# Performance work log

Measured on AMD Instinct MI355X. Metric: run time of the kernel, lower is better.

The kernel has to match this reference:

```python
import math
import jax, jax.numpy as jnp
import numpy as np

H = 1024        # hidden_size
V = 32000       # target vocab
T = 64          # decoder steps
B = 32          # batch
NL = 2          # lstm layers
WSZ = 50        # window_size
WLEN = 2 * WSZ + 1
L = 128         # source length (all sequences full)
S = L + WLEN    # padded encoder length, guarantees windows in-bounds
HH = math.ceil(H / 2)
STD2 = (WSZ / 2.0) ** 2
EPS = 1e-14


def setup_inputs():
    key = jax.random.key(0)
    ks = jax.random.split(key, 16)
    sc = 0.02
    inp = {}
    inp["encoder_output"] = jax.random.normal(ks[0], (S, B, H), jnp.float32)
    inp["context"] = jax.random.normal(ks[1], (T, B, H), jnp.float32)
    inp["h0"] = jax.random.normal(ks[2], (NL, B, H), jnp.float32)
    inp["c0"] = jax.random.normal(ks[3], (NL, B, H), jnp.float32)
    inp["embedding"] = jax.random.normal(ks[4], (V, H), jnp.float32) * sc
    inp["attn_w1"] = jax.random.normal(ks[5], (HH, H), jnp.float32) * sc
    inp["attn_b1"] = jnp.zeros((HH,), jnp.float32)
    inp["attn_w2"] = jax.random.normal(ks[6], (1, HH), jnp.float32) * sc
    inp["attn_b2"] = jnp.zeros((1,), jnp.float32)
    inp["lstm_Wih0"] = jax.random.normal(ks[7], (4 * H, 2 * H), jnp.float32) * sc  # input feeding: 2H input
    inp["lstm_Whh0"] = jax.random.normal(ks[8], (4 * H, H), jnp.float32) * sc
    inp["lstm_bih0"] = jnp.zeros((4 * H,), jnp.float32)
    inp["lstm_bhh0"] = jnp.zeros((4 * H,), jnp.float32)
    inp["lstm_Wih1"] = jax.random.normal(ks[9], (4 * H, H), jnp.float32) * sc
    inp["lstm_Whh1"] = jax.random.normal(ks[10], (4 * H, H), jnp.float32) * sc
    inp["lstm_bih1"] = jnp.zeros((4 * H,), jnp.float32)
    inp["lstm_bhh1"] = jnp.zeros((4 * H,), jnp.float32)
    inp["fc1_w"] = jax.random.normal(ks[11], (H, 2 * H), jnp.float32) * sc
    inp["fc1_b"] = jnp.zeros((H,), jnp.float32)
    inp["fc2_w"] = jax.random.normal(ks[12], (V, H), jnp.float32) * sc
    inp["fc2_b"] = jnp.zeros((V,), jnp.float32)
    inp["target_words"] = jax.random.randint(ks[13], (T, B), 0, V)
    inp["lengths"] = jnp.full((B,), L, dtype=jnp.int32)
    return inp


def _lstm_layer(x, h0, c0, Wih, Whh, bih, bhh):
    bias = bih + bhh
    def step(carry, xt):
        h, c = carry
        gates = xt @ Wih.T + h @ Whh.T + bias   # [B, 4H], torch gate order i,f,g,o
        i, f, g, o = jnp.split(gates, 4, axis=-1)
        c = jax.nn.sigmoid(f) * c + jax.nn.sigmoid(i) * jnp.tanh(g)
        h = jax.nn.sigmoid(o) * jnp.tanh(c)
        return (h, c), h
    (hT, cT), ys = jax.lax.scan(step, (h0, c0), x)
    return ys, hT, cT


def _attention(encoder_output, dec_out, lengths, aw1, ab1, aw2, ab2):
    h_s = jnp.transpose(encoder_output, (1, 0, 2))   # [B, S, H]
    h_t = jnp.transpose(dec_out, (1, 0, 2))          # [B, T, H]
    p = jax.nn.sigmoid(jnp.tanh(h_t @ aw1.T + ab1) @ aw2.T + ab2)[..., 0]  # [B, T]
    p = WSZ + lengths[:, None].astype(jnp.float32) * p
    win_start = jnp.round(p - WSZ).astype(jnp.int32)                        # [B, T]
    k = jnp.arange(WLEN)
    positions = win_start[..., None].astype(jnp.float32) + k.astype(jnp.float32)  # [B, T, W]
    gaussian = jnp.exp(-((positions - p[..., None]) ** 2) / (2.0 * STD2))
    # faithful to original: the selection buffer is overwritten every j, so
    # every decoder step attends over the LAST step's window
    sel_idx = win_start[:, -1][:, None] + k                                 # [B, W]
    selection = jnp.take_along_axis(h_s, sel_idx[:, :, None], axis=1)       # [B, W, H]
    score = jnp.einsum('bth,bwh->btw', h_t, selection)
    li = lengths[:, None, None].astype(jnp.int32)
    lo = k[None, None, :] < (WSZ - win_start)[..., None]
    hi = k[None, None, :] >= (li + WSZ - win_start[..., None])
    score = jnp.where(lo | hi, EPS, score)   # original writes epsilon, NOT -inf
    a = jax.nn.softmax(score, axis=2) * gaussian
    c = jnp.einsum('btw,bwh->bth', a, selection)
    return jnp.transpose(c, (1, 0, 2))       # [T, B, H]


def reference(encoder_output, context, h0, c0, embedding,
              attn_w1, attn_b1, attn_w2, attn_b2,
              lstm_Wih0, lstm_Whh0, lstm_bih0, lstm_bhh0,
              lstm_Wih1, lstm_Whh1, lstm_bih1, lstm_bhh1,
              fc1_w, fc1_b, fc2_w, fc2_b,
              target_words, lengths):
    emb = embedding[target_words]                        # [T, B, H]
    x = jnp.concatenate([emb, context], axis=2)          # input feeding -> [T, B, 2H]
    y0, hT0, cT0 = _lstm_layer(x, h0[0], c0[0], lstm_Wih0, lstm_Whh0, lstm_bih0, lstm_bhh0)
    y1, hT1, cT1 = _lstm_layer(y0, h0[1], c0[1], lstm_Wih1, lstm_Whh1, lstm_bih1, lstm_bhh1)
    ctx = _attention(encoder_output, y1, lengths, attn_w1, attn_b1, attn_w2, attn_b2)
    out = jax.nn.relu(jnp.concatenate([ctx, y1], axis=2) @ fc1_w.T + fc1_b)
    y = out @ fc2_w.T + fc2_b                            # [T, B, V]
    h_n = jnp.stack([hT0, hT1])
    c_n = jnp.stack([cT0, cT1])
    return (y, h_n, c_n, ctx)
```

## Files before the change

kernel.cpp:

```cpp
#include <hip/hip_runtime.h>
#include <hip/hip_bf16.h>

#define T_STEPS 64
#define BATCH   32
#define HID     1024
#define VOCAB   32000
#define WLEN_   101
#define WSZ_    50
#define SENC    229
#define LBLK    64

static const size_t Y_SZ   = (size_t)T_STEPS * BATCH * VOCAB;
static const size_t HN_SZ  = (size_t)2 * BATCH * HID;
static const size_t CTX_OFF = Y_SZ + 2 * HN_SZ;

typedef __attribute__((ext_vector_type(8)))  unsigned short us8;
typedef __attribute__((ext_vector_type(8)))  __bf16 bf16x8;
typedef __attribute__((ext_vector_type(4)))  float f32x4;
typedef __attribute__((ext_vector_type(16))) float f32x16;

static __device__ inline unsigned short f2bf(float x) {
    __hip_bfloat16 b = __float2bfloat16(x);
    return __builtin_bit_cast(unsigned short, b);
}

#define GLD_US8_SC(dst, ptr) \
    asm volatile("global_load_dwordx4 %0, %1, off sc0 sc1" : "=v"(dst) : "v"(ptr) : "memory")
#define GLD_F32_SC(dst, ptr) \
    asm volatile("global_load_dword %0, %1, off sc0 sc1" : "=v"(dst) : "v"(ptr) : "memory")
#define GST_U16_SC(ptr, val) \
    asm volatile("global_store_short %0, %1, off sc0 sc1" :: "v"(ptr), "v"(val) : "memory")
#define GST_U32_SC(ptr, val) \
    asm volatile("global_store_dword %0, %1, off sc0 sc1" :: "v"(ptr), "v"(val) : "memory")
#define WAIT_VM0() asm volatile("s_waitcnt vmcnt(0)" ::: "memory")

__global__ __launch_bounds__(256) void gemm_bt(
    const float* __restrict__ A, const float* __restrict__ W,
    const float* __restrict__ b1, const float* __restrict__ b2,
    float* __restrict__ out, int M, int N, int K, int act)
{
    __shared__ __align__(16) float As[16 * 132];
    __shared__ __align__(16) float Ws[16 * 68];
    const int tid  = threadIdx.x;
    const int col0 = blockIdx.x * 64;
    const int row0 = blockIdx.y * 128;
    const int ty   = tid >> 4;
    const int tx   = tid & 15;

    float acc[8][4];
#pragma unroll
    for (int i = 0; i < 8; ++i)
#pragma unroll
        for (int j = 0; j < 4; ++j) acc[i][j] = 0.f;

    for (int k0 = 0; k0 < K; k0 += 16) {
#pragma unroll
        for (int li = 0; li < 2; ++li) {
            int f  = tid + li * 256;
            int r  = f >> 2;
            int kq = (f & 3) << 2;
            float4 v = *reinterpret_cast<const float4*>(A + (size_t)(row0 + r) * K + k0 + kq);
            As[(kq + 0) * 132 + r] = v.x;
            As[(kq + 1) * 132 + r] = v.y;
            As[(kq + 2) * 132 + r] = v.z;
            As[(kq + 3) * 132 + r] = v.w;
        }
        {
            int n  = tid >> 2;
            int kq = (tid & 3) << 2;
            float4 v = *reinterpret_cast<const float4*>(W + (size_t)(col0 + n) * K + k0 + kq);
            Ws[(kq + 0) * 68 + n] = v.x;
            Ws[(kq + 1) * 68 + n] = v.y;
            Ws[(kq + 2) * 68 + n] = v.z;
            Ws[(kq + 3) * 68 + n] = v.w;
        }
        __syncthreads();
#pragma unroll
        for (int k = 0; k < 16; ++k) {
            const float4 a0 = *reinterpret_cast<const float4*>(&As[k * 132 + ty * 8]);
            const float4 a1 = *reinterpret_cast<const float4*>(&As[k * 132 + ty * 8 + 4]);
            const float4 b0 = *reinterpret_cast<const float4*>(&Ws[k * 68 + tx * 4]);
            float av[8] = {a0.x, a0.y, a0.z, a0.w, a1.x, a1.y, a1.z, a1.w};
            float bv[4] = {b0.x, b0.y, b0.z, b0.w};
#pragma unroll
            for (int i = 0; i < 8; ++i)
#pragma unroll
                for (int j = 0; j < 4; ++j) acc[i][j] = fmaf(av[i], bv[j], acc[i][j]);
        }
        __syncthreads();
    }

#pragma unroll
    for (int j = 0; j < 4; ++j) {
        int n = col0 + tx * 4 + j;
        float bias = 0.f;
        if (b1) bias += b1[n];
        if (b2) bias += b2[n];
#pragma unroll
        for (int i = 0; i < 8; ++i) {
            float v = acc[i][j] + bias;
            if (act == 1) v = fmaxf(v, 0.f);
            else if (act == 2) v = tanhf(v);
            out[(size_t)(row0 + ty * 8 + i) * N + n] = v;
        }
    }
}

__global__ __launch_bounds__(256) void gemm_lds_bt(
    const unsigned short* __restrict__ A, const unsigned short* __restrict__ W,
    const float* __restrict__ b1, const float* __restrict__ b2,
    float* __restrict__ out, unsigned short* __restrict__ out_bf,
    int M, int N, int K, int relu)
{
    __shared__ __align__(16) unsigned short As[8192];
    __shared__ __align__(16) unsigned short Ws[8192];
    const int tid  = threadIdx.x;
    const int lane = tid & 63;
    const int wave = tid >> 6;

    const int nwg = gridDim.x;
    const int bid = blockIdx.x;
    const int q = nwg >> 3, r8 = nwg & 7;
    const int xcd = bid & 7, sidx = bid >> 3;
    const int wgid = (xcd < r8 ? xcd * (q + 1) : r8 * (q + 1) + (xcd - r8) * q) + sidx;
    const int mt = M >> 7;
    const int row0 = (wgid % mt) << 7;
    const int col0 = (wgid / mt) << 7;

    const int m0   = (wave >> 1) * 64;
    const int n0   = (wave & 1) * 64;
    const int lrow = lane & 15;
    const int kc   = lane >> 4;

    f32x4 acc[4][4];
#pragma unroll
    for (int i = 0; i < 4; ++i)
#pragma unroll
        for (int j = 0; j < 4; ++j) acc[i][j] = (f32x4){0.f, 0.f, 0.f, 0.f};

    const bool isA = (wave < 2);
    const int  lw  = wave & 1;
    const unsigned short* gbase = isA ? (A + (size_t)row0 * K) : (W + (size_t)col0 * K);
    unsigned short* lbase = isA ? As : Ws;

    for (int k0 = 0; k0 < K; k0 += 64) {
#pragma unroll
        for (int i = 0; i < 8; ++i) {
            const int c    = lw * 512 + i * 64 + lane;
            const int row  = c >> 3;
            const int slot = c & 7;
            const unsigned short* src =
                gbase + (size_t)row * K + k0 + ((slot ^ (row & 7)) << 3);
            __builtin_amdgcn_global_load_lds(
                (const __attribute__((address_space(1))) void*)src,
                (__attribute__((address_space(3))) void*)(lbase + (size_t)(lw * 512 + i * 64) * 8),
                16, 0, 0);
        }
        __syncthreads();
#pragma unroll
        for (int ss = 0; ss < 2; ++ss) {
            us8 a[4], b[4];
#pragma unroll
            for (int f = 0; f < 4; ++f) {
                const int ar = m0 + f * 16 + lrow;
                const int as = (ss * 4 + kc) ^ (ar & 7);
                a[f] = *reinterpret_cast<const us8*>(&As[(ar * 8 + as) * 8]);
                const int br = n0 + f * 16 + lrow;
                const int bs = (ss * 4 + kc) ^ (br & 7);
                b[f] = *reinterpret_cast<const us8*>(&Ws[(br * 8 + bs) * 8]);
            }
#pragma unroll
            for (int fi = 0; fi < 4; ++fi)
#pragma unroll
                for (int fj = 0; fj < 4; ++fj)
                    acc[fi][fj] = __builtin_amdgcn_mfma_f32_16x16x32_bf16(
                        __builtin_bit_cast(bf16x8, a[fi]),
                        __builtin_bit_cast(bf16x8, b[fj]),
                        acc[fi][fj], 0, 0, 0);
        }
        __syncthreads();
    }

#pragma unroll
    for (int fi = 0; fi < 4; ++fi)
#pragma unroll
        for (int fj = 0; fj < 4; ++fj) {
            const int cN = col0 + n0 + fj * 16 + lrow;
            float bv = 0.f;
            if (b1) bv += b1[cN];
            if (b2) bv += b2[cN];
#pragma unroll
            for (int j = 0; j < 4; ++j) {
                const int r = row0 + m0 + fi * 16 + (lane >> 4) * 4 + j;
                float v = acc[fi][fj][j] + bv;
                if (relu) v = fmaxf(v, 0.f);
                if (out)    out[(size_t)r * N + cN] = v;
                if (out_bf) out_bf[(size_t)r * N + cN] = f2bf(v);
            }
        }
}

__global__ void cvt_bf16_kernel(const float* __restrict__ src,
                                unsigned short* __restrict__ dst, int n8)
{
    for (int i = blockIdx.x * blockDim.x + threadIdx.x; i < n8;
         i += gridDim.x * blockDim.x) {
        float4 v0 = *reinterpret_cast<const float4*>(src + (size_t)i * 8);
        float4 v1 = *reinterpret_cast<const float4*>(src + (size_t)i * 8 + 4);
        us8 c = {f2bf(v0.x), f2bf(v0.y), f2bf(v0.z), f2bf(v0.w),
                 f2bf(v1.x), f2bf(v1.y), f2bf(v1.z), f2bf(v1.w)};
        *reinterpret_cast<us8*>(dst + (size_t)i * 8) = c;
    }
}

__global__ void embed_concat_bf_kernel(const float* __restrict__ emb,
                                       const float* __restrict__ ctxin,
                                       const int* __restrict__ tw,
                                       unsigned short* __restrict__ x_bf)
{
    const int total = 2048 * 256;
    for (int idx = blockIdx.x * blockDim.x + threadIdx.x; idx < total;
         idx += gridDim.x * blockDim.x) {
        int row = idx >> 8;
        int c8  = idx & 255;
        const float* src = (c8 < 128)
            ? emb + (size_t)tw[row] * HID + c8 * 8
            : ctxin + (size_t)row * HID + (c8 - 128) * 8;
        float4 v0 = *reinterpret_cast<const float4*>(src);
        float4 v1 = *reinterpret_cast<const float4*>(src + 4);
        us8 c = {f2bf(v0.x), f2bf(v0.y), f2bf(v0.z), f2bf(v0.w),
                 f2bf(v1.x), f2bf(v1.y), f2bf(v1.z), f2bf(v1.w)};
        *reinterpret_cast<us8*>(x_bf + (size_t)idx * 8) = c;
    }
}

__global__ void zero_flags_kernel(int* p, int n)
{
    int i = blockIdx.x * blockDim.x + threadIdx.x;
    if (i < n) p[i] = 0;
}

static __device__ inline void hier_arrive(int* __restrict__ flags, int phase, int tid)
{
    if (tid == 0)
        __hip_atomic_store(&flags[blockIdx.x * 32], phase,
                           __ATOMIC_RELAXED, __HIP_MEMORY_SCOPE_AGENT);
}

static __device__ inline void hier_wait(int* __restrict__ flags, int* __restrict__ epoch,
                                        int phase, int tid)
{
    if (blockIdx.x == 0) {
        if (tid < 3 * LBLK) {
            while (__hip_atomic_load(&flags[tid * 32], __ATOMIC_RELAXED,
                                     __HIP_MEMORY_SCOPE_AGENT) < phase)
                __builtin_amdgcn_s_sleep(1);
        }
        __syncthreads();
        if (tid < 8)
            __hip_atomic_store(&epoch[tid * 32], phase,
                               __ATOMIC_RELAXED, __HIP_MEMORY_SCOPE_AGENT);
    } else {
        if (tid == 0) {
            const int slot = (blockIdx.x & 7) * 32;
            while (__hip_atomic_load(&epoch[slot], __ATOMIC_RELAXED,
                                     __HIP_MEMORY_SCOPE_AGENT) < phase)
                __builtin_amdgcn_s_sleep(1);
        }
        __syncthreads();
    }
}

__global__ __launch_bounds__(256) void lstm_fused3(
    const float* __restrict__ gpre0,
    const float* __restrict__ Whh0, const float* __restrict__ Wih1,
    const float* __restrict__ Whh1,
    const float* __restrict__ bih1, const float* __restrict__ bhh1,
    const float* __restrict__ h0all, const float* __restrict__ c0all,
    float* __restrict__ y1o,
    unsigned short* __restrict__ fin_bf,
    float* __restrict__ hn, float* __restrict__ cn,
    unsigned short* __restrict__ hbf,
    float* __restrict__ part,
    int* __restrict__ flags, int* __restrict__ epoch,
    const float* __restrict__ fc2w, unsigned short* __restrict__ fc2w_bf,
    int foldcvt)
{
    __shared__ __align__(16) us8 WB[8192];
    __shared__ float red2[32 * 132];
    __shared__ float csh[512];

    const int tid  = threadIdx.x;
    const int lane = tid & 63;
    const int w    = tid >> 6;
    const int n    = lane & 31;
    const int kh   = lane >> 5;
    const int bid  = blockIdx.x;
    const int role = bid >> 6;
    const int lb   = bid & 63;
    const int j0   = lb * 16;
    const int b    = tid >> 3;
    const int jj   = tid & 7;

    unsigned short* hb0 = hbf;
    unsigned short* hb1 = hbf + 65536;

    {
        const float* Wsrc = (role == 0) ? Whh0 : (role == 1 ? Wih1 : Whh1);
        const int g = n >> 3, cj = n & 7;
#pragma unroll
        for (int T = 0; T < 2; ++T) {
            const float* wrow = Wsrc + (size_t)(g * HID + j0 + T * 8 + cj) * HID;
#pragma unroll
            for (int f = 0; f < 16; ++f) {
                int k = w * 256 + f * 16 + kh * 8;
                float4 v0 = *reinterpret_cast<const float4*>(wrow + k);
                float4 v1 = *reinterpret_cast<const float4*>(wrow + k + 4);
                WB[((T * 4 + w) * 16 + f) * 64 + lane] =
                    (us8){f2bf(v0.x), f2bf(v0.y), f2bf(v0.z), f2bf(v0.w),
                          f2bf(v1.x), f2bf(v1.y), f2bf(v1.z), f2bf(v1.w)};
            }
        }
    }

    float gp[2][4] = {};
    float bb[2][4] = {};
    if (role == 0) {
#pragma unroll
        for (int T = 0; T < 2; ++T) {
            csh[T * 256 + tid] = c0all[b * HID + j0 + T * 8 + jj];
#pragma unroll
            for (int g = 0; g < 4; ++g)
                gp[T][g] = gpre0[(size_t)b * 4096 + g * HID + j0 + T * 8 + jj];
        }
#pragma unroll
        for (int q = 0; q < 2; ++q) {
            int e = lb * 512 + q * 256 + tid;
            unsigned int hv = f2bf(h0all[((e >> 3) & 31) * HID + (e >> 8) * 8 + (e & 7)]);
            GST_U16_SC(hb0 + e, hv);
        }
    } else if (role == 2) {
#pragma unroll
        for (int T = 0; T < 2; ++T) {
            csh[T * 256 + tid] = c0all[32768 + b * HID + j0 + T * 8 + jj];
#pragma unroll
            for (int g = 0; g < 4; ++g)
                bb[T][g] = bih1[g * HID + j0 + T * 8 + jj] + bhh1[g * HID + j0 + T * 8 + jj];
        }
#pragma unroll
        for (int q = 0; q < 2; ++q) {
            int e = lb * 512 + q * 256 + tid;
            unsigned int hv = f2bf(h0all[32768 + ((e >> 3) & 31) * HID + (e >> 8) * 8 + (e & 7)]);
            GST_U16_SC(hb1 + 32768 + e, hv);
        }
    }

    WAIT_VM0();
    __syncthreads();
    hier_arrive(flags, 1, tid);
    hier_wait(flags, epoch, 1, tid);

    for (int p = 0; p <= 65; ++p) {
        const bool active = (role == 0) ? (p <= 63)
                          : (role == 1) ? (p >= 1 && p <= 64)
                                        : (p >= 2);
        if (active) {
            const int t = p - role;
            float pv[2][4];
            if (role == 2) {
                const float* pb = part + (size_t)(p & 1) * 131072 + lb * 2048 + tid;
#pragma unroll
                for (int T = 0; T < 2; ++T)
#pragma unroll
                    for (int g = 0; g < 4; ++g)
                        GLD_F32_SC(pv[T][g], pb + (T * 4 + g) * 256);
            }
            const unsigned short* hsrc = (role == 2)
                ? hb1 + ((p + 1) & 1) * 32768
                : hb0 + (p & 1) * 32768;
            const unsigned short* hr = hsrc + (size_t)w * 8192 + lane * 8;
            us8 aF[16];
#pragma unroll
            for (int f = 0; f < 16; ++f)
                GLD_US8_SC(aF[f], hr + f * 512);
            WAIT_VM0();
            __builtin_amdgcn_sched_barrier(0);

            f32x16 acc0 = {}, acc1 = {};
#pragma unroll
            for (int f = 0; f < 16; ++f)
                acc0 = __builtin_amdgcn_mfma_f32_32x32x16_bf16(
                    __builtin_bit_cast(bf16x8, aF[f]),
                    __builtin_bit_cast(bf16x8, WB[((0 * 4 + w) * 16 + f) * 64 + lane]),
                    acc0, 0, 0, 0);
#pragma unroll
            for (int f = 0; f < 16; ++f)
                acc1 = __builtin_amdgcn_mfma_f32_32x32x16_bf16(
                    __builtin_bit_cast(bf16x8, aF[f]),
                    __builtin_bit_cast(bf16x8, WB[((1 * 4 + w) * 16 + f) * 64 + lane]),
                    acc1, 0, 0, 0);

#pragma unroll
            for (int T = 0; T < 2; ++T) {
                if (T == 1) __syncthreads();
#pragma unroll
                for (int r = 0; r < 16; ++r) {
                    int m = (r & 3) + 8 * (r >> 2) + 4 * kh;
                    red2[m * 132 + w * 32 + n] = (T == 0) ? acc0[r] : acc1[r];
                }
                __syncthreads();
                float s0, s1, s2, s3;
                {
                    const float* rr = &red2[b * 132 + jj];
                    s0 = rr[0]  + rr[32]  + rr[64]  + rr[96];
                    s1 = rr[8]  + rr[40]  + rr[72]  + rr[104];
                    s2 = rr[16] + rr[48]  + rr[80]  + rr[112];
                    s3 = rr[24] + rr[56]  + rr[88]  + rr[120];
                }
                const int col = j0 + T * 8 + jj;
                const int he  = (lb * 2 + T) * 256 + tid;
                if (role == 1) {
                    float* pdst = part + (size_t)((p - 1) & 1) * 131072 + lb * 2048 + tid;
                    GST_U32_SC(pdst + (T * 4 + 0) * 256, s0);
                    GST_U32_SC(pdst + (T * 4 + 1) * 256, s1);
                    GST_U32_SC(pdst + (T * 4 + 2) * 256, s2);
                    GST_U32_SC(pdst + (T * 4 + 3) * 256, s3);
                } else {
                    if (role == 0) { s0 += gp[T][0]; s1 += gp[T][1]; s2 += gp[T][2]; s3 += gp[T][3]; }
                    else { s0 += pv[T][0] + bb[T][0]; s1 += pv[T][1] + bb[T][1];
                           s2 += pv[T][2] + bb[T][2]; s3 += pv[T][3] + bb[T][3]; }
                    float ig = 1.f / (1.f + expf(-s0));
                    float fg = 1.f / (1.f + expf(-s1));
                    float gg = tanhf(s2);
                    float og = 1.f / (1.f + expf(-s3));
                    float cv = fg * csh[T * 256 + tid] + ig * gg;
                    csh[T * 256 + tid] = cv;
                    float h = og * tanhf(cv);
                    unsigned int hv = f2bf(h);
                    if (role == 0) {
                        GST_U16_SC(hb0 + ((p + 1) & 1) * 32768 + he, hv);
                        if (t == T_STEPS - 1) { hn[b * HID + col] = h; cn[b * HID + col] = cv; }
                    } else {
                        __builtin_nontemporal_store(h, &y1o[(size_t)t * 32768 + b * HID + col]);
                        fin_bf[(size_t)(t * BATCH + b) * 2048 + 1024 + col] = f2bf(h);
                        if (t == T_STEPS - 1) {
                            hn[32768 + b * HID + col] = h;
                            cn[32768 + b * HID + col] = cv;
                        } else {
                            GST_U16_SC(hb1 + (p & 1) * 32768 + he, hv);
                        }
                    }
                }
            }
        }
        if (p < 65) {
            WAIT_VM0();
            __syncthreads();
            hier_arrive(flags, p + 2, tid);
            if (role == 0 && p + 1 <= 63) {
                const float* gsrc = gpre0 + (size_t)((p + 1) * BATCH + b) * 4096 + j0 + jj;
#pragma unroll
                for (int T = 0; T < 2; ++T)
#pragma unroll
                    for (int g = 0; g < 4; ++g)
                        gp[T][g] = gsrc[g * HID + T * 8];
            }
            if (foldcvt && p < 64 && bid != 0) {
                const int slot = p * 191 + (bid - 1);
                for (int j = tid; j < 336; j += 256) {
                    int i = slot * 336 + j;
                    if (i < 4096000) {
                        float4 v0 = *reinterpret_cast<const float4*>(fc2w + (size_t)i * 8);
                        float4 v1 = *reinterpret_cast<const float4*>(fc2w + (size_t)i * 8 + 4);
                        us8 c = {f2bf(v0.x), f2bf(v0.y), f2bf(v0.z), f2bf(v0.w),
                                 f2bf(v1.x), f2bf(v1.y), f2bf(v1.z), f2bf(v1.w)};
                        *reinterpret_cast<us8*>(fc2w_bf + (size_t)i * 8) = c;
                    }
                }
            }
            hier_wait(flags, epoch, p + 2, tid);
        }
    }
}

__global__ __launch_bounds__(64) void attn_p_kernel(
    const float* __restrict__ hidden1, const float* __restrict__ aw2,
    const float* __restrict__ ab2, const int* __restrict__ lengths,
    float* __restrict__ p_arr, int* __restrict__ win_arr)
{
    const int row = blockIdx.x;
    const int lane = threadIdx.x;
    float s = 0.f;
    for (int i = lane; i < 512; i += 64) s += hidden1[(size_t)row * 512 + i] * aw2[i];
    for (int off = 32; off > 0; off >>= 1) s += __shfl_down(s, off);
    if (lane == 0) {
        float v = s + ab2[0];
        float sig = 1.f / (1.f + expf(-v));
        int b = row & 31;
        float lf = (float)lengths[b];
        p_arr[row] = (float)WSZ_ + lf * sig;
        win_arr[row] = (int)rintf(lf * sig);
    }
}

__global__ __launch_bounds__(128) void attn_fused_kernel(
    const float* __restrict__ y1, const float* __restrict__ enc,
    const float* __restrict__ p_arr, const int* __restrict__ win_arr,
    const int* __restrict__ lengths, float* __restrict__ ctx,
    unsigned short* __restrict__ fin_bf)
{
    __shared__ __align__(16) float yl[1024];
    __shared__ float sv[WLEN_];
    __shared__ float av[WLEN_];
    const int row = blockIdx.x;
    const int b   = row & 31;
    const int tid = threadIdx.x;

    for (int i = tid; i < 1024; i += 128) yl[i] = y1[(size_t)row * HID + i];
    __syncthreads();

    const int win = win_arr[row];
    const int wl  = win_arr[(T_STEPS - 1) * BATCH + b];
    const float p = p_arr[row];
    const int len = lengths[b];

    if (tid < WLEN_) {
        const float4* s4 = reinterpret_cast<const float4*>(
            enc + ((size_t)(wl + tid) * BATCH + b) * HID);
        const float4* y4 = reinterpret_cast<const float4*>(yl);
        float acc = 0.f;
        for (int q = 0; q < 256; ++q) {
            float4 a = s4[q]; float4 yy = y4[q];
            acc += a.x * yy.x + a.y * yy.y + a.z * yy.z + a.w * yy.w;
        }
        bool lo = tid < (WSZ_ - win);
        bool hi = tid >= (len + WSZ_ - win);
        sv[tid] = (lo || hi) ? 1e-14f : acc;
    }
    __syncthreads();

    float mx = -1e30f;
    for (int w = 0; w < WLEN_; ++w) mx = fmaxf(mx, sv[w]);
    float sum = 0.f;
    for (int w = 0; w < WLEN_; ++w) sum += expf(sv[w] - mx);
    if (tid < WLEN_) {
        float e = expf(sv[tid] - mx) / sum;
        float d = (float)(win + tid) - p;
        av[tid] = e * expf(-(d * d) / 1250.f);
    }
    __syncthreads();

    float acc[8] = {0, 0, 0, 0, 0, 0, 0, 0};
    for (int w = 0; w < WLEN_; ++w) {
        float a = av[w];
        const float* srow = enc + ((size_t)(wl + w) * BATCH + b) * HID;
#pragma unroll
        for (int i = 0; i < 8; ++i) acc[i] += a * srow[tid + 128 * i];
    }
    for (int i = 0; i < 8; ++i) {
        ctx[(size_t)row * HID + tid + 128 * i] = acc[i];
        fin_bf[(size_t)row * 2048 + tid + 128 * i] = f2bf(acc[i]);
    }
}

extern "C" void kernel_launch(void* const* d_in, const int* in_sizes, int n_in,
                              void* d_out, int out_size, void* d_ws, size_t ws_size,
                              hipStream_t stream)
{
    const float* enc   = (const float*)d_in[0];
    const float* ctxin = (const float*)d_in[1];
    const float* h0    = (const float*)d_in[2];
    const float* c0    = (const float*)d_in[3];
    const float* emb   = (const float*)d_in[4];
    const float* aw1   = (const float*)d_in[5];
    const float* ab1   = (const float*)d_in[6];
    const float* aw2   = (const float*)d_in[7];
    const float* ab2   = (const float*)d_in[8];
    const float* Wih0  = (const float*)d_in[9];
    const float* Whh0  = (const float*)d_in[10];
    const float* bih0  = (const float*)d_in[11];
    const float* bhh0  = (const float*)d_in[12];
    const float* Wih1  = (const float*)d_in[13];
    const float* Whh1  = (const float*)d_in[14];
    const float* bih1  = (const float*)d_in[15];
    const float* bhh1  = (const float*)d_in[16];
    const float* fc1w  = (const float*)d_in[17];
    const float* fc1b  = (const float*)d_in[18];
    const float* fc2w  = (const float*)d_in[19];
    const float* fc2b  = (const float*)d_in[20];
    const int*   tw    = (const int*)d_in[21];
    const int*   lens  = (const int*)d_in[22];

    float* ws = (float*)d_ws;
    float*          buf_gates = ws;
    unsigned short* x_bf      = (unsigned short*)(ws + 8388608);
    float*          buf_part  = ws + 8388608;
    unsigned short* Wih0_bf   = (unsigned short*)(ws + 10485760);
    float*          buf_y1    = ws + 16384000;
    unsigned short* buf_hbf   = (unsigned short*)(ws + 18481152);
    int*            buf_flags = (int*)(ws + 18546688);
    int*            buf_epoch = buf_flags + 8192;
    float*          buf_hidden1 = ws + 18555136;
    float*          buf_p     = ws + 19603712;
    int*            buf_win   = (int*)(ws + 19605760);
    unsigned short* fin_bf    = (unsigned short*)(ws + 22917376);
    unsigned short* fc1w_bf   = (unsigned short*)(ws + 25014528);
    unsigned short* fc1out_bf = (unsigned short*)(ws + 26063104);

    const size_t fold_end_bytes = (size_t)(27111680 + 8192000) * 4;
    const int foldcvt = (ws_size >= fold_end_bytes) ? 1 : 0;
    unsigned short* fc2w_bf = foldcvt ? (unsigned short*)(ws + 27111680)
                                      : (unsigned short*)ws;

    float* out   = (float*)d_out;
    float* out_hn  = out + Y_SZ;
    float* out_cn  = out + Y_SZ + HN_SZ;
    float* out_ctx = out + CTX_OFF;

    zero_flags_kernel<<<33, 256, 0, stream>>>(buf_flags, 8448);
    cvt_bf16_kernel<<<2048, 256, 0, stream>>>(Wih0, Wih0_bf, 4096 * 2048 / 8);
    cvt_bf16_kernel<<<1024, 256, 0, stream>>>(fc1w, fc1w_bf, 1024 * 2048 / 8);
    embed_concat_bf_kernel<<<2048, 256, 0, stream>>>(emb, ctxin, tw, x_bf);

    gemm_lds_bt<<<512, 256, 0, stream>>>(
        x_bf, Wih0_bf, bih0, bhh0, buf_gates, nullptr, 2048, 4096, 2048, 0);

    lstm_fused3<<<3 * LBLK, 256, 0, stream>>>(
        buf_gates, Whh0, Wih1, Whh1, bih1, bhh1, h0, c0,
        buf_y1, fin_bf, out_hn, out_cn, buf_hbf, buf_part,
        buf_flags, buf_epoch, fc2w, fc2w_bf, foldcvt);

    if (!foldcvt)
        cvt_bf16_kernel<<<2048, 256, 0, stream>>>(fc2w, fc2w_bf, VOCAB * HID / 8);

    gemm_bt<<<dim3(512 / 64, 2048 / 128), 256, 0, stream>>>(
        buf_y1, aw1, ab1, nullptr, buf_hidden1, 2048, 512, 1024, 2 );
    attn_p_kernel<<<2048, 64, 0, stream>>>(buf_hidden1, aw2, ab2, lens, buf_p, buf_win);
    attn_fused_kernel<<<2048, 128, 0, stream>>>(buf_y1, enc, buf_p, buf_win, lens,
                                                out_ctx, fin_bf);

    gemm_lds_bt<<<128, 256, 0, stream>>>(
        fin_bf, fc1w_bf, fc1b, nullptr, nullptr, fc1out_bf, 2048, 1024, 2048, 1);

    gemm_lds_bt<<<4000, 256, 0, stream>>>(
        fc1out_bf, fc2w_bf, fc2b, nullptr, out, nullptr, 2048, VOCAB, 1024, 0);
}
```

Before: 936.2 us.

## Replace global grid barrier with per-role dependency epochs in fused LSTM

The single hierarchical barrier across all 192 blocks of the persistent LSTM kernel is replaced by three per-role epoch counters (layer-0, layer-1 input, layer-1 recurrent). Each block now waits only on the producer roles it depends on. The h and partial-sum ring buffers grow from 2 to 4 slots so roles can run ahead of one another without overwriting data still being read. The fc2 weight conversion folded into the loop is moved off the critical role-0 blocks onto role-1 and role-2 blocks. The intent is to cut barrier latency and let the pipeline stages drift apart, at the cost of more complex lag reasoning and a larger workspace.

```diff
diff --git a/kernel.cpp b/kernel.cpp
--- a/kernel.cpp
+++ b/kernel.cpp
@@ -240,35 +240,45 @@
     if (i < n) p[i] = 0;
 }
 
-static __device__ inline void hier_arrive(int* __restrict__ flags, int phase, int tid)
-{
-    if (tid == 0)
-        __hip_atomic_store(&flags[blockIdx.x * 32], phase,
-                           __ATOMIC_RELAXED, __HIP_MEMORY_SCOPE_AGENT);
-}
-
-static __device__ inline void hier_wait(int* __restrict__ flags, int* __restrict__ epoch,
-                                        int phase, int tid)
-{
-    if (blockIdx.x == 0) {
-        if (tid < 3 * LBLK) {
-            while (__hip_atomic_load(&flags[tid * 32], __ATOMIC_RELAXED,
-                                     __HIP_MEMORY_SCOPE_AGENT) < phase)
+static __device__ inline void dep_wait(int* __restrict__ flags, int role, int lb,
+                                       int q, int tid)
+{
+    int* epA = flags + 6144;
+    int* epC = flags + 6400;
+    int* epB = flags + 6656;
+    if (lb == 0) {
+        if (tid < 64) {
+            const int fi = (role * 64 + tid) * 32;
+            while (__hip_atomic_load(&flags[fi], __ATOMIC_RELAXED,
+                                     __HIP_MEMORY_SCOPE_AGENT) < q + 1)
                 __builtin_amdgcn_s_sleep(1);
         }
         __syncthreads();
+        int* ep = (role == 0) ? epA : (role == 1 ? epC : epB);
         if (tid < 8)
-            __hip_atomic_store(&epoch[tid * 32], phase,
+            __hip_atomic_store(&ep[tid * 32], q + 1,
                                __ATOMIC_RELAXED, __HIP_MEMORY_SCOPE_AGENT);
-    } else {
-        if (tid == 0) {
-            const int slot = (blockIdx.x & 7) * 32;
-            while (__hip_atomic_load(&epoch[slot], __ATOMIC_RELAXED,
-                                     __HIP_MEMORY_SCOPE_AGENT) < phase)
-                __builtin_amdgcn_s_sleep(1);
-        }
-        __syncthreads();
-    }
+    }
+    int* e1; int t1; int* e2; int t2;
+    if (role == 0)      { e1 = epA; t1 = q + 1; e2 = epC; t2 = q - 1; }
+    else if (role == 1) { e1 = epA; t1 = q + 1; e2 = epB; t2 = q - 1; }
+    else                { e1 = epC; t1 = q + 1; e2 = epB; t2 = q + 1; }
+    if (lb == 0) {
+        if (role == 0) e1 = nullptr;
+        else if (role == 2) e2 = nullptr;
+    }
+    const int slot = ((int)blockIdx.x & 7) * 32;
+    if (tid == 0 && e1) {
+        while (__hip_atomic_load(&e1[slot], __ATOMIC_RELAXED,
+                                 __HIP_MEMORY_SCOPE_AGENT) < t1)
+            __builtin_amdgcn_s_sleep(1);
+    }
+    if (tid == 64 && e2 && t2 > 1) {
+        while (__hip_atomic_load(&e2[slot], __ATOMIC_RELAXED,
+                                 __HIP_MEMORY_SCOPE_AGENT) < t2)
+            __builtin_amdgcn_s_sleep(1);
+    }
+    __syncthreads();
 }
 
 __global__ __launch_bounds__(256) void lstm_fused3(
@@ -282,7 +292,7 @@
     float* __restrict__ hn, float* __restrict__ cn,
     unsigned short* __restrict__ hbf,
     float* __restrict__ part,
-    int* __restrict__ flags, int* __restrict__ epoch,
+    int* __restrict__ flags,
     const float* __restrict__ fc2w, unsigned short* __restrict__ fc2w_bf,
     int foldcvt)
 {
@@ -303,7 +313,7 @@
     const int jj   = tid & 7;
 
     unsigned short* hb0 = hbf;
-    unsigned short* hb1 = hbf + 65536;
+    unsigned short* hb1 = hbf + 131072;
 
     {
         const float* Wsrc = (role == 0) ? Whh0 : (role == 1 ? Wih1 : Whh1);
@@ -357,10 +367,11 @@
 
     WAIT_VM0();
     __syncthreads();
-    hier_arrive(flags, 1, tid);
-    hier_wait(flags, epoch, 1, tid);
+    if (tid == 0)
+        __hip_atomic_store(&flags[bid * 32], 1, __ATOMIC_RELAXED, __HIP_MEMORY_SCOPE_AGENT);
 
     for (int p = 0; p <= 65; ++p) {
+        dep_wait(flags, role, lb, p, tid);
         const bool active = (role == 0) ? (p <= 63)
                           : (role == 1) ? (p >= 1 && p <= 64)
                                         : (p >= 2);
@@ -368,7 +379,7 @@
             const int t = p - role;
             float pv[2][4];
             if (role == 2) {
-                const float* pb = part + (size_t)(p & 1) * 131072 + lb * 2048 + tid;
+                const float* pb = part + (size_t)((p - 2) & 3) * 131072 + lb * 2048 + tid;
 #pragma unroll
                 for (int T = 0; T < 2; ++T)
 #pragma unroll
@@ -377,7 +388,7 @@
             }
             const unsigned short* hsrc = (role == 2)
                 ? hb1 + ((p + 1) & 1) * 32768
-                : hb0 + (p & 1) * 32768;
+                : hb0 + (p & 3) * 32768;
             const unsigned short* hr = hsrc + (size_t)w * 8192 + lane * 8;
             us8 aF[16];
 #pragma unroll
@@ -420,7 +431,7 @@
                 const int col = j0 + T * 8 + jj;
                 const int he  = (lb * 2 + T) * 256 + tid;
                 if (role == 1) {
-                    float* pdst = part + (size_t)((p - 1) & 1) * 131072 + lb * 2048 + tid;
+                    float* pdst = part + (size_t)((p - 1) & 3) * 131072 + lb * 2048 + tid;
                     GST_U32_SC(pdst + (T * 4 + 0) * 256, s0);
                     GST_U32_SC(pdst + (T * 4 + 1) * 256, s1);
                     GST_U32_SC(pdst + (T * 4 + 2) * 256, s2);
@@ -438,7 +449,7 @@
                     float h = og * tanhf(cv);
                     unsigned int hv = f2bf(h);
                     if (role == 0) {
-                        GST_U16_SC(hb0 + ((p + 1) & 1) * 32768 + he, hv);
+                        GST_U16_SC(hb0 + ((p + 1) & 3) * 32768 + he, hv);
                         if (t == T_STEPS - 1) { hn[b * HID + col] = h; cn[b * HID + col] = cv; }
                     } else {
                         __builtin_nontemporal_store(h, &y1o[(size_t)t * 32768 + b * HID + col]);
@@ -456,7 +467,9 @@
         if (p < 65) {
             WAIT_VM0();
             __syncthreads();
-            hier_arrive(flags, p + 2, tid);
+            if (tid == 0)
+                __hip_atomic_store(&flags[bid * 32], p + 2,
+                                   __ATOMIC_RELAXED, __HIP_MEMORY_SCOPE_AGENT);
             if (role == 0 && p + 1 <= 63) {
                 const float* gsrc = gpre0 + (size_t)((p + 1) * BATCH + b) * 4096 + j0 + jj;
 #pragma unroll
@@ -465,10 +478,11 @@
                     for (int g = 0; g < 4; ++g)
                         gp[T][g] = gsrc[g * HID + T * 8];
             }
-            if (foldcvt && p < 64 && bid != 0) {
-                const int slot = p * 191 + (bid - 1);
-                for (int j = tid; j < 336; j += 256) {
-                    int i = slot * 336 + j;
+            if (foldcvt && p < 64 && bid >= 64 && bid != 64 && bid != 128) {
+                const int cidx = (bid < 128) ? (bid - 65) : (63 + bid - 129);
+                const int base = (p * 126 + cidx) * 508;
+                for (int j = tid; j < 508; j += 256) {
+                    int i = base + j;
                     if (i < 4096000) {
                         float4 v0 = *reinterpret_cast<const float4*>(fc2w + (size_t)i * 8);
                         float4 v1 = *reinterpret_cast<const float4*>(fc2w + (size_t)i * 8 + 4);
@@ -478,7 +492,6 @@
                     }
                 }
             }
-            hier_wait(flags, epoch, p + 2, tid);
         }
     }
 }
@@ -598,11 +611,10 @@
     unsigned short* Wih0_bf   = (unsigned short*)(ws + 10485760);
     float*          buf_y1    = ws + 16384000;
     unsigned short* buf_hbf   = (unsigned short*)(ws + 18481152);
-    int*            buf_flags = (int*)(ws + 18546688);
-    int*            buf_epoch = buf_flags + 8192;
-    float*          buf_hidden1 = ws + 18555136;
-    float*          buf_p     = ws + 19603712;
-    int*            buf_win   = (int*)(ws + 19605760);
+    int*            buf_flags = (int*)(ws + 18579456);
+    float*          buf_hidden1 = ws + 18587904;
+    float*          buf_p     = ws + 19636480;
+    int*            buf_win   = (int*)(ws + 19638528);
     unsigned short* fin_bf    = (unsigned short*)(ws + 22917376);
     unsigned short* fc1w_bf   = (unsigned short*)(ws + 25014528);
     unsigned short* fc1out_bf = (unsigned short*)(ws + 26063104);
@@ -628,7 +640,7 @@
     lstm_fused3<<<3 * LBLK, 256, 0, stream>>>(
         buf_gates, Whh0, Wih1, Whh1, bih1, bhh1, h0, c0,
         buf_y1, fin_bf, out_hn, out_cn, buf_hbf, buf_part,
-        buf_flags, buf_epoch, fc2w, fc2w_bf, foldcvt);
+        buf_flags, fc2w, fc2w_bf, foldcvt);
 
     if (!foldcvt)
         cvt_bf16_kernel<<<2048, 256, 0, stream>>>(fc2w, fc2w_bf, VOCAB * HID / 8);
```

New measurement: 956.1 us. 1.02x slower.
